# Kernel optimization log

Measured on AMD Instinct MI355X. Metric: run time of the kernel, lower is better.

## Reference

```python
import jax, jax.numpy as jnp
import numpy as np

E = 100000   # num edges
N = 50000    # num nodes (eg_idx, v, t triples)
B = 64       # num queries / subgraphs
D = 128      # n_dims_in
ID = 4 * D   # concat of 4 embeddings
OD = 2 * D   # G output dims
K = 1000     # max_edges per eg_idx


def setup_inputs() -> dict:
    key = jax.random.key(0)
    ks = jax.random.split(key, 12)
    eg_idx = jnp.sort(jax.random.randint(ks[0], (E,), 0, B)).astype(jnp.int32)
    node_i = jax.random.randint(ks[1], (E,), 0, N).astype(jnp.int32)
    node_j = jax.random.randint(ks[2], (E,), 0, N).astype(jnp.int32)
    node_score = jax.random.uniform(ks[3], (N,), dtype=jnp.float32)
    memorized_embedding = jax.random.normal(ks[4], (N, D), dtype=jnp.float32)
    rel_emb = jax.random.normal(ks[5], (E, D), dtype=jnp.float32)
    query_src_ts_emb = jax.random.normal(ks[6], (B, D), dtype=jnp.float32)
    query_rel_emb = jax.random.normal(ks[7], (B, D), dtype=jnp.float32)
    # G params: left/right dense init ~ N(0, sqrt(2/in)), center xavier-ish
    Wl = jax.random.normal(ks[8], (ID, OD), dtype=jnp.float32) * np.sqrt(2.0 / ID)
    Wr = jax.random.normal(ks[9], (ID, OD), dtype=jnp.float32) * np.sqrt(2.0 / ID)
    Wc = jax.random.normal(ks[10], (OD, OD), dtype=jnp.float32) * np.sqrt(2.0 / (OD + OD))
    bl = jnp.zeros((OD,), jnp.float32)
    br = jnp.zeros((OD,), jnp.float32)
    bc = jnp.zeros((OD,), jnp.float32)
    return dict(eg_idx=eg_idx, node_i=node_i, node_j=node_j, node_score=node_score,
                memorized_embedding=memorized_embedding, rel_emb=rel_emb,
                query_src_ts_emb=query_src_ts_emb, query_rel_emb=query_rel_emb,
                Wl=Wl, bl=bl, Wr=Wr, br=br, Wc=Wc, bc=bc, k=K)


def _segment_softmax(logits, seg, num_segments):
    m = jax.ops.segment_max(logits, seg, num_segments=num_segments)
    e = jnp.exp(logits - m[seg])
    s = jax.ops.segment_sum(e, seg, num_segments=num_segments)
    return e / s[seg]


def _topk_keep_mask(scores, group, num_groups, k):
    # keep edge iff its score ranks < k within its group (per-eg_idx topk)
    n = scores.shape[0]
    order = jnp.lexsort((-scores, group))          # sort by group asc, score desc
    sorted_group = group[order]
    counts = jax.ops.segment_sum(jnp.ones((n,), jnp.int32), group, num_segments=num_groups)
    starts = jnp.cumsum(counts) - counts           # exclusive cumsum: group start offsets
    rank_in_group = jnp.arange(n) - starts[sorted_group]
    keep_sorted = rank_in_group < k
    return jnp.zeros((n,), bool).at[order].set(keep_sorted)


def reference(eg_idx, node_i, node_j, node_score, memorized_embedding, rel_emb,
              query_src_ts_emb, query_rel_emb, Wl, bl, Wr, br, Wc, bc, k):
    num_nodes = memorized_embedding.shape[0]
    num_groups = query_src_ts_emb.shape[0]
    # gather per-edge embeddings
    hvi = memorized_embedding[node_i]              # [E, D]
    hvj = memorized_embedding[node_j]
    q_src = query_src_ts_emb[eg_idx]               # [E, D]
    q_rel = query_rel_emb[eg_idx]
    # G: bilinear MLP attention
    left_x = jnp.concatenate([hvi, rel_emb, q_src, q_rel], axis=-1)   # [E, 4D]
    right_x = jnp.concatenate([hvj, rel_emb, q_src, q_rel], axis=-1)
    l = jax.nn.leaky_relu(left_x @ Wl + bl)                           # [E, 2D]
    r = jax.nn.leaky_relu(right_x @ Wr + br) @ Wc + bc
    transition_logits = jnp.sum(l * r, axis=-1)                       # [E]
    # segment softmax over source node (eg_idx, vi, ti)
    soft = _segment_softmax(transition_logits, node_i, num_nodes)
    src_att = node_score[node_i]
    target_att = soft * src_att
    # per-eg_idx top-k pruning (keep mask instead of ragged slicing)
    keep = _topk_keep_mask(target_att, eg_idx, num_groups, k).astype(target_att.dtype)
    # sum aggregation: scatter soft * target_att into target nodes over kept edges
    updated_node_score = jax.ops.segment_sum(keep * soft * target_att, node_j,
                                             num_segments=num_nodes)
    return updated_node_score
```

## Files before the change

kernel.cpp:

```cpp
#include <hip/hip_runtime.h>

#define DD   128
#define ODIM 256
#define TE   32
#define TSLICE 16

__device__ __forceinline__ float leaky(float v) { return v > 0.f ? v : 0.01f * v; }

__global__ void k_query(const float* __restrict__ qs, const float* __restrict__ qr,
                        const float* __restrict__ Wl, const float* __restrict__ bl,
                        const float* __restrict__ Wr, const float* __restrict__ br,
                        float* __restrict__ Ql, float* __restrict__ Qr)
{
    const int g = blockIdx.x, t = threadIdx.x;
    float al = bl[t], ar = br[t];
    const float* qsg = qs + (size_t)g * DD;
    const float* qrg = qr + (size_t)g * DD;
    for (int k = 0; k < DD; ++k) {
        float a = qsg[k], b = qrg[k];
        al = fmaf(a, Wl[(size_t)(256 + k) * ODIM + t], al);
        al = fmaf(b, Wl[(size_t)(384 + k) * ODIM + t], al);
        ar = fmaf(a, Wr[(size_t)(256 + k) * ODIM + t], ar);
        ar = fmaf(b, Wr[(size_t)(384 + k) * ODIM + t], ar);
    }
    Ql[(size_t)g * ODIM + t] = al;
    Qr[(size_t)g * ODIM + t] = ar;
}

#define FMA4(dst, xc, wv, j)                                \
    dst[j][0] = fmaf(xc, wv.x, dst[j][0]);                  \
    dst[j][1] = fmaf(xc, wv.y, dst[j][1]);                  \
    dst[j][2] = fmaf(xc, wv.z, dst[j][2]);                  \
    dst[j][3] = fmaf(xc, wv.w, dst[j][3]);


__global__ __launch_bounds__(256, 2)
void k_nodepre(const float* __restrict__ me, const float* __restrict__ Wl,
               const float* __restrict__ Wr, float* __restrict__ Xl,
               float* __restrict__ Xr, int N)
{
    __shared__ float s_me[TE][DD];

    const int tx   = threadIdx.x;
    const int wave = tx >> 6;
    const int lane = tx & 63;
    const int colg = lane & 15;
    const int edgeg= lane >> 4;
    const int c0   = wave * 64 + colg * 4;
    const int eb   = edgeg * 8;
    const int n0   = blockIdx.x * TE;

    for (int it = tx; it < TE * DD / 4; it += 256) {
        int i  = it >> 5;
        int k4 = it & 31;
        float4 h = make_float4(0.f, 0.f, 0.f, 0.f);
        if (n0 + i < N) h = *(const float4*)(me + (size_t)(n0 + i) * DD + 4 * k4);
        *(float4*)(&s_me[i][(k4 ^ ((i >> 3) & 3)) << 2]) = h;
    }
    __syncthreads();

    float acc[8][4];
#pragma unroll
    for (int j = 0; j < 8; ++j) { acc[j][0] = acc[j][1] = acc[j][2] = acc[j][3] = 0.f; }
    for (int k4 = 0; k4 < 32; ++k4) {
        const float* wp = Wl + (size_t)(4 * k4) * ODIM + c0;
        float4 w0 = *(const float4*)(wp);
        float4 w1 = *(const float4*)(wp + ODIM);
        float4 w2 = *(const float4*)(wp + 2 * ODIM);
        float4 w3 = *(const float4*)(wp + 3 * ODIM);
        const int pc = (k4 ^ edgeg) << 2;
#pragma unroll
        for (int j = 0; j < 8; ++j) {
            float4 x = *(const float4*)(&s_me[eb + j][pc]);
            FMA4(acc, x.x, w0, j) FMA4(acc, x.y, w1, j) FMA4(acc, x.z, w2, j) FMA4(acc, x.w, w3, j)
        }
    }
#pragma unroll
    for (int j = 0; j < 8; ++j) {
        int n = n0 + eb + j;
        if (n < N)
            *(float4*)(Xl + (size_t)n * ODIM + c0) = make_float4(acc[j][0], acc[j][1], acc[j][2], acc[j][3]);
    }

#pragma unroll
    for (int j = 0; j < 8; ++j) { acc[j][0] = acc[j][1] = acc[j][2] = acc[j][3] = 0.f; }
    for (int k4 = 0; k4 < 32; ++k4) {
        const float* wp = Wr + (size_t)(4 * k4) * ODIM + c0;
        float4 w0 = *(const float4*)(wp);
        float4 w1 = *(const float4*)(wp + ODIM);
        float4 w2 = *(const float4*)(wp + 2 * ODIM);
        float4 w3 = *(const float4*)(wp + 3 * ODIM);
        const int pc = (k4 ^ edgeg) << 2;
#pragma unroll
        for (int j = 0; j < 8; ++j) {
            float4 x = *(const float4*)(&s_me[eb + j][pc]);
            FMA4(acc, x.x, w0, j) FMA4(acc, x.y, w1, j) FMA4(acc, x.z, w2, j) FMA4(acc, x.w, w3, j)
        }
    }
#pragma unroll
    for (int j = 0; j < 8; ++j) {
        int n = n0 + eb + j;
        if (n < N)
            *(float4*)(Xr + (size_t)n * ODIM + c0) = make_float4(acc[j][0], acc[j][1], acc[j][2], acc[j][3]);
    }
}

__global__ __launch_bounds__(256, 2)
void k_edge_logits_pre(const int* __restrict__ eg_idx, const int* __restrict__ node_i,
                       const int* __restrict__ node_j, const float* __restrict__ rel,
                       const float* __restrict__ Wl, const float* __restrict__ Wr,
                       const float* __restrict__ Wc, const float* __restrict__ bc,
                       const float* __restrict__ Ql, const float* __restrict__ Qr,
                       const float* __restrict__ Xl, const float* __restrict__ Xr,
                       float* __restrict__ logits, int E)
{
    __shared__ float s_a[TE][DD];
    __shared__ float s_b[TE][DD];
    __shared__ float s_red[4][TE];
    __shared__ int   s_ni[TE], s_nj[TE], s_g[TE];

    const int tx   = threadIdx.x;
    const int wave = tx >> 6;
    const int lane = tx & 63;
    const int colg = lane & 15;
    const int edgeg= lane >> 4;
    const int c0   = wave * 64 + colg * 4;
    const int eb   = edgeg * 8;
    const int e0   = blockIdx.x * TE;

    if (tx < TE) {
        int e = e0 + tx;
        s_ni[tx] = (e < E) ? node_i[e] : 0;
        s_nj[tx] = (e < E) ? node_j[e] : 0;
        s_g[tx]  = (e < E) ? eg_idx[e] : 0;
    }
    __syncthreads();

    for (int it = tx; it < TE * DD / 4; it += 256) {
        int i  = it >> 5;
        int k4 = it & 31;
        float4 v = make_float4(0.f, 0.f, 0.f, 0.f);
        if (e0 + i < E) v = *(const float4*)(rel + (size_t)(e0 + i) * DD + 4 * k4);
        *(float4*)(&s_a[i][(k4 ^ ((i >> 3) & 3)) << 2]) = v;
    }
    __syncthreads();

    float acc[8][4];
#pragma unroll
    for (int j = 0; j < 8; ++j) { acc[j][0] = acc[j][1] = acc[j][2] = acc[j][3] = 0.f; }

    for (int k4 = 0; k4 < 32; ++k4) {
        const float* wp = Wr + (size_t)(DD + 4 * k4) * ODIM + c0;
        float4 w0 = *(const float4*)(wp);
        float4 w1 = *(const float4*)(wp + ODIM);
        float4 w2 = *(const float4*)(wp + 2 * ODIM);
        float4 w3 = *(const float4*)(wp + 3 * ODIM);
        const int pc = (k4 ^ edgeg) << 2;
#pragma unroll
        for (int j = 0; j < 8; ++j) {
            float4 x = *(const float4*)(&s_a[eb + j][pc]);
            FMA4(acc, x.x, w0, j) FMA4(acc, x.y, w1, j) FMA4(acc, x.z, w2, j) FMA4(acc, x.w, w3, j)
        }
    }

#pragma unroll
    for (int j = 0; j < 8; ++j) {
        float4 xr = *(const float4*)(Xr + (size_t)s_nj[eb + j] * ODIM + c0);
        float4 q  = *(const float4*)(Qr + (size_t)s_g[eb + j] * ODIM + c0);
        acc[j][0] = leaky(acc[j][0] + xr.x + q.x);
        acc[j][1] = leaky(acc[j][1] + xr.y + q.y);
        acc[j][2] = leaky(acc[j][2] + xr.z + q.z);
        acc[j][3] = leaky(acc[j][3] + xr.w + q.w);
    }

    float uacc[8][4];
#pragma unroll
    for (int j = 0; j < 8; ++j) { uacc[j][0] = uacc[j][1] = uacc[j][2] = uacc[j][3] = 0.f; }

    if (wave < 2) {
        const int pc = ((wave * 16 + colg) ^ edgeg) << 2;
#pragma unroll
        for (int j = 0; j < 8; ++j)
            *(float4*)(&s_b[eb + j][pc]) = make_float4(acc[j][0], acc[j][1], acc[j][2], acc[j][3]);
    }
    __syncthreads();
    for (int k4 = 0; k4 < 32; ++k4) {
        const float* wp = Wc + (size_t)(4 * k4) * ODIM + c0;
        float4 w0 = *(const float4*)(wp);
        float4 w1 = *(const float4*)(wp + ODIM);
        float4 w2 = *(const float4*)(wp + 2 * ODIM);
        float4 w3 = *(const float4*)(wp + 3 * ODIM);
        const int pc = (k4 ^ edgeg) << 2;
#pragma unroll
        for (int j = 0; j < 8; ++j) {
            float4 x = *(const float4*)(&s_b[eb + j][pc]);
            FMA4(uacc, x.x, w0, j) FMA4(uacc, x.y, w1, j) FMA4(uacc, x.z, w2, j) FMA4(uacc, x.w, w3, j)
        }
    }
    __syncthreads();
    if (wave >= 2) {
        const int pc = ((wave * 16 + colg - 32) ^ edgeg) << 2;
#pragma unroll
        for (int j = 0; j < 8; ++j)
            *(float4*)(&s_b[eb + j][pc]) = make_float4(acc[j][0], acc[j][1], acc[j][2], acc[j][3]);
    }
    __syncthreads();
    for (int k4 = 0; k4 < 32; ++k4) {
        const float* wp = Wc + (size_t)(DD + 4 * k4) * ODIM + c0;
        float4 w0 = *(const float4*)(wp);
        float4 w1 = *(const float4*)(wp + ODIM);
        float4 w2 = *(const float4*)(wp + 2 * ODIM);
        float4 w3 = *(const float4*)(wp + 3 * ODIM);
        const int pc = (k4 ^ edgeg) << 2;
#pragma unroll
        for (int j = 0; j < 8; ++j) {
            float4 x = *(const float4*)(&s_b[eb + j][pc]);
            FMA4(uacc, x.x, w0, j) FMA4(uacc, x.y, w1, j) FMA4(uacc, x.z, w2, j) FMA4(uacc, x.w, w3, j)
        }
    }

    {
        float4 bcv = *(const float4*)(bc + c0);
#pragma unroll
        for (int j = 0; j < 8; ++j) {
            uacc[j][0] += bcv.x; uacc[j][1] += bcv.y;
            uacc[j][2] += bcv.z; uacc[j][3] += bcv.w;
        }
    }

#pragma unroll
    for (int j = 0; j < 8; ++j) { acc[j][0] = acc[j][1] = acc[j][2] = acc[j][3] = 0.f; }
    for (int k4 = 0; k4 < 32; ++k4) {
        const float* wp = Wl + (size_t)(DD + 4 * k4) * ODIM + c0;
        float4 w0 = *(const float4*)(wp);
        float4 w1 = *(const float4*)(wp + ODIM);
        float4 w2 = *(const float4*)(wp + 2 * ODIM);
        float4 w3 = *(const float4*)(wp + 3 * ODIM);
        const int pc = (k4 ^ edgeg) << 2;
#pragma unroll
        for (int j = 0; j < 8; ++j) {
            float4 x = *(const float4*)(&s_a[eb + j][pc]);
            FMA4(acc, x.x, w0, j) FMA4(acc, x.y, w1, j) FMA4(acc, x.z, w2, j) FMA4(acc, x.w, w3, j)
        }
    }

#pragma unroll
    for (int j = 0; j < 8; ++j) {
        float4 xl = *(const float4*)(Xl + (size_t)s_ni[eb + j] * ODIM + c0);
        float4 q  = *(const float4*)(Ql + (size_t)s_g[eb + j] * ODIM + c0);
        float p = leaky(acc[j][0] + xl.x + q.x) * uacc[j][0]
                + leaky(acc[j][1] + xl.y + q.y) * uacc[j][1]
                + leaky(acc[j][2] + xl.z + q.z) * uacc[j][2]
                + leaky(acc[j][3] + xl.w + q.w) * uacc[j][3];
        p += __shfl_xor(p, 1);
        p += __shfl_xor(p, 2);
        p += __shfl_xor(p, 4);
        p += __shfl_xor(p, 8);
        if (colg == 0) s_red[wave][eb + j] = p;
    }
    __syncthreads();
    if (tx < TE) {
        int e = e0 + tx;
        if (e < E)
            logits[e] = s_red[0][tx] + s_red[1][tx] + s_red[2][tx] + s_red[3][tx];
    }
}

__global__ __launch_bounds__(256, 2)
void k_edge_logits(const int* __restrict__ eg_idx, const int* __restrict__ node_i,
                   const int* __restrict__ node_j,
                   const float* __restrict__ me, const float* __restrict__ rel,
                   const float* __restrict__ Wl, const float* __restrict__ Wr,
                   const float* __restrict__ Wc, const float* __restrict__ bc,
                   const float* __restrict__ Ql, const float* __restrict__ Qr,
                   float* __restrict__ logits, int E)
{
    __shared__ float s_a[TE][DD];
    __shared__ float s_b[TE][DD];
    __shared__ int   s_ni[TE], s_nj[TE], s_g[TE];

    const int tx = threadIdx.x;
    const int cg = tx & 63;
    const int er = tx >> 6;
    const int c0 = cg << 2;
    const int e0 = blockIdx.x * TE;
    const int eb = er * 8;

    if (tx < TE) {
        int e = e0 + tx;
        s_ni[tx] = (e < E) ? node_i[e] : 0;
        s_nj[tx] = (e < E) ? node_j[e] : 0;
        s_g[tx]  = (e < E) ? eg_idx[e] : 0;
    }
    __syncthreads();

    for (int it = tx; it < TE * DD / 4; it += 256) {
        int i  = it >> 5;
        int kk = (it & 31) << 2;
        float4 v = make_float4(0.f, 0.f, 0.f, 0.f);
        float4 h = v;
        if (e0 + i < E) {
            v = *(const float4*)(rel + (size_t)(e0 + i) * DD + kk);
            h = *(const float4*)(me + (size_t)s_nj[i] * DD + kk);
        }
        *(float4*)(&s_a[i][kk]) = v;
        *(float4*)(&s_b[i][kk]) = h;
    }
    __syncthreads();

    float acc[8][4];
#pragma unroll
    for (int j = 0; j < 8; ++j) { acc[j][0] = acc[j][1] = acc[j][2] = acc[j][3] = 0.f; }

    for (int k = 0; k < DD; k += 4) {
        const float* wp = Wr + (size_t)k * ODIM + c0;
        float4 w0 = *(const float4*)(wp);
        float4 w1 = *(const float4*)(wp + ODIM);
        float4 w2 = *(const float4*)(wp + 2 * ODIM);
        float4 w3 = *(const float4*)(wp + 3 * ODIM);
#pragma unroll
        for (int j = 0; j < 8; ++j) {
            float4 x = *(const float4*)(&s_b[eb + j][k]);
            FMA4(acc, x.x, w0, j) FMA4(acc, x.y, w1, j) FMA4(acc, x.z, w2, j) FMA4(acc, x.w, w3, j)
        }
    }
    for (int k = 0; k < DD; k += 4) {
        const float* wp = Wr + (size_t)(DD + k) * ODIM + c0;
        float4 w0 = *(const float4*)(wp);
        float4 w1 = *(const float4*)(wp + ODIM);
        float4 w2 = *(const float4*)(wp + 2 * ODIM);
        float4 w3 = *(const float4*)(wp + 3 * ODIM);
#pragma unroll
        for (int j = 0; j < 8; ++j) {
            float4 x = *(const float4*)(&s_a[eb + j][k]);
            FMA4(acc, x.x, w0, j) FMA4(acc, x.y, w1, j) FMA4(acc, x.z, w2, j) FMA4(acc, x.w, w3, j)
        }
    }

#pragma unroll
    for (int j = 0; j < 8; ++j) {
        int g = s_g[eb + j];
        float4 q = *(const float4*)(Qr + (size_t)g * ODIM + c0);
        acc[j][0] = leaky(acc[j][0] + q.x);
        acc[j][1] = leaky(acc[j][1] + q.y);
        acc[j][2] = leaky(acc[j][2] + q.z);
        acc[j][3] = leaky(acc[j][3] + q.w);
    }

    float uacc[8][4];
#pragma unroll
    for (int j = 0; j < 8; ++j) { uacc[j][0] = uacc[j][1] = uacc[j][2] = uacc[j][3] = 0.f; }

    __syncthreads();
    if (c0 < DD) {
#pragma unroll
        for (int j = 0; j < 8; ++j)
            *(float4*)(&s_b[eb + j][c0]) = make_float4(acc[j][0], acc[j][1], acc[j][2], acc[j][3]);
    }
    __syncthreads();
    for (int k = 0; k < DD; k += 4) {
        const float* wp = Wc + (size_t)k * ODIM + c0;
        float4 w0 = *(const float4*)(wp);
        float4 w1 = *(const float4*)(wp + ODIM);
        float4 w2 = *(const float4*)(wp + 2 * ODIM);
        float4 w3 = *(const float4*)(wp + 3 * ODIM);
#pragma unroll
        for (int j = 0; j < 8; ++j) {
            float4 x = *(const float4*)(&s_b[eb + j][k]);
            FMA4(uacc, x.x, w0, j) FMA4(uacc, x.y, w1, j) FMA4(uacc, x.z, w2, j) FMA4(uacc, x.w, w3, j)
        }
    }
    __syncthreads();
    if (c0 >= DD) {
#pragma unroll
        for (int j = 0; j < 8; ++j)
            *(float4*)(&s_b[eb + j][c0 - DD]) = make_float4(acc[j][0], acc[j][1], acc[j][2], acc[j][3]);
    }
    __syncthreads();
    for (int k = 0; k < DD; k += 4) {
        const float* wp = Wc + (size_t)(DD + k) * ODIM + c0;
        float4 w0 = *(const float4*)(wp);
        float4 w1 = *(const float4*)(wp + ODIM);
        float4 w2 = *(const float4*)(wp + 2 * ODIM);
        float4 w3 = *(const float4*)(wp + 3 * ODIM);
#pragma unroll
        for (int j = 0; j < 8; ++j) {
            float4 x = *(const float4*)(&s_b[eb + j][k]);
            FMA4(uacc, x.x, w0, j) FMA4(uacc, x.y, w1, j) FMA4(uacc, x.z, w2, j) FMA4(uacc, x.w, w3, j)
        }
    }

    {
        float4 bcv = *(const float4*)(bc + c0);
#pragma unroll
        for (int j = 0; j < 8; ++j) {
            uacc[j][0] += bcv.x; uacc[j][1] += bcv.y;
            uacc[j][2] += bcv.z; uacc[j][3] += bcv.w;
        }
    }

    __syncthreads();
    for (int it = tx; it < TE * DD / 4; it += 256) {
        int i  = it >> 5;
        int kk = (it & 31) << 2;
        float4 h = make_float4(0.f, 0.f, 0.f, 0.f);
        if (e0 + i < E) h = *(const float4*)(me + (size_t)s_ni[i] * DD + kk);
        *(float4*)(&s_b[i][kk]) = h;
    }
    __syncthreads();

#pragma unroll
    for (int j = 0; j < 8; ++j) { acc[j][0] = acc[j][1] = acc[j][2] = acc[j][3] = 0.f; }

    for (int k = 0; k < DD; k += 4) {
        const float* wp = Wl + (size_t)k * ODIM + c0;
        float4 w0 = *(const float4*)(wp);
        float4 w1 = *(const float4*)(wp + ODIM);
        float4 w2 = *(const float4*)(wp + 2 * ODIM);
        float4 w3 = *(const float4*)(wp + 3 * ODIM);
#pragma unroll
        for (int j = 0; j < 8; ++j) {
            float4 x = *(const float4*)(&s_b[eb + j][k]);
            FMA4(acc, x.x, w0, j) FMA4(acc, x.y, w1, j) FMA4(acc, x.z, w2, j) FMA4(acc, x.w, w3, j)
        }
    }
    for (int k = 0; k < DD; k += 4) {
        const float* wp = Wl + (size_t)(DD + k) * ODIM + c0;
        float4 w0 = *(const float4*)(wp);
        float4 w1 = *(const float4*)(wp + ODIM);
        float4 w2 = *(const float4*)(wp + 2 * ODIM);
        float4 w3 = *(const float4*)(wp + 3 * ODIM);
#pragma unroll
        for (int j = 0; j < 8; ++j) {
            float4 x = *(const float4*)(&s_a[eb + j][k]);
            FMA4(acc, x.x, w0, j) FMA4(acc, x.y, w1, j) FMA4(acc, x.z, w2, j) FMA4(acc, x.w, w3, j)
        }
    }

#pragma unroll
    for (int j = 0; j < 8; ++j) {
        int g = s_g[eb + j];
        float4 q = *(const float4*)(Ql + (size_t)g * ODIM + c0);
        float p = leaky(acc[j][0] + q.x) * uacc[j][0]
                + leaky(acc[j][1] + q.y) * uacc[j][1]
                + leaky(acc[j][2] + q.z) * uacc[j][2]
                + leaky(acc[j][3] + q.w) * uacc[j][3];
#pragma unroll
        for (int off = 32; off > 0; off >>= 1) p += __shfl_down(p, off);
        if (cg == 0) {
            int e = e0 + eb + j;
            if (e < E) logits[e] = p;
        }
    }
}

__device__ __forceinline__ unsigned f32_enc(float f) {
    unsigned u = __float_as_uint(f);
    return (u & 0x80000000u) ? ~u : (u | 0x80000000u);
}
__device__ __forceinline__ float f32_dec(unsigned x) {
    return (x & 0x80000000u) ? __uint_as_float(x & 0x7fffffffu) : __uint_as_float(~x);
}

__global__ void k_segmax(const float* __restrict__ logits, const int* __restrict__ ni,
                         unsigned* __restrict__ segmax, int E)
{
    int e = blockIdx.x * 256 + threadIdx.x;
    if (e >= E) return;
    atomicMax(&segmax[ni[e]], f32_enc(logits[e]));
}

__global__ void k_expsum(const float* __restrict__ logits, const int* __restrict__ ni,
                         const unsigned* __restrict__ segmax,
                         float* __restrict__ eexp, float* __restrict__ segsum, int E)
{
    int e = blockIdx.x * 256 + threadIdx.x;
    if (e >= E) return;
    float m = f32_dec(segmax[ni[e]]);
    float v = expf(logits[e] - m);
    eexp[e] = v;
    atomicAdd(&segsum[ni[e]], v);
}

__global__ void k_soft(const float* __restrict__ eexp, const float* __restrict__ segsum,
                       const int* __restrict__ ni, const float* __restrict__ node_score,
                       float* __restrict__ soft, float* __restrict__ ta, int E)
{
    int e = blockIdx.x * 256 + threadIdx.x;
    if (e >= E) return;
    int n = ni[e];
    float s = eexp[e] / segsum[n];
    soft[e] = s;
    ta[e]   = s * node_score[n];
}

__global__ void k_starts(const int* __restrict__ eg, int E, int B, int* __restrict__ starts)
{
    int g = blockIdx.x * blockDim.x + threadIdx.x;
    if (g > B) return;
    int lo = 0, hi = E;
    while (lo < hi) { int mid = (lo + hi) >> 1; if (eg[mid] < g) lo = mid + 1; else hi = mid; }
    starts[g] = lo;
}

__global__ __launch_bounds__(256)
void k_topk(const int* __restrict__ starts, const int* __restrict__ node_j,
            const float* __restrict__ soft, const float* __restrict__ ta,
            const int* __restrict__ kptr, float* __restrict__ out)
{
    __shared__ float s_val[2048];
    const int g  = blockIdx.x / TSLICE;
    const int sl = blockIdx.x % TSLICE;
    const int gs = starts[g], ge = starts[g + 1];
    const int cnt = ge - gs;
    if (cnt <= 0) return;
    const int per = (cnt + TSLICE - 1) / TSLICE;
    const int c0  = sl * per;
    const int c1  = min(cnt, c0 + per);
    if (c0 >= cnt) return;
    const int K  = kptr[0];
    const int tx = threadIdx.x;

    for (int base = c0; base < c1; base += 256) {
        int   li  = base + tx;
        bool  act = li < c1;
        float mv  = act ? ta[gs + li] : 0.f;
        int   rank = 0;
        for (int t0 = 0; t0 < cnt; t0 += 2048) {
            int tlen = min(2048, cnt - t0);
            __syncthreads();
            for (int i = tx; i < tlen; i += 256) s_val[i] = ta[gs + t0 + i];
            __syncthreads();
            for (int i = 0; i < tlen; ++i) {
                float v  = s_val[i];
                int   gi = t0 + i;
                rank += (int)((v > mv) || (v == mv && gi < li));
            }
        }
        if (act && rank < K) {
            int e = gs + li;
            atomicAdd(&out[node_j[e]], soft[e] * ta[e]);
        }
    }
}

extern "C" void kernel_launch(void* const* d_in, const int* in_sizes, int n_in,
                              void* d_out, int out_size, void* d_ws, size_t ws_size,
                              hipStream_t stream)
{
    const int*   eg_idx     = (const int*)d_in[0];
    const int*   node_i     = (const int*)d_in[1];
    const int*   node_j     = (const int*)d_in[2];
    const float* node_score = (const float*)d_in[3];
    const float* me         = (const float*)d_in[4];
    const float* rel        = (const float*)d_in[5];
    const float* qs         = (const float*)d_in[6];
    const float* qr         = (const float*)d_in[7];
    const float* Wl         = (const float*)d_in[8];
    const float* bl         = (const float*)d_in[9];
    const float* Wr         = (const float*)d_in[10];
    const float* br         = (const float*)d_in[11];
    const float* Wc         = (const float*)d_in[12];
    const float* bc         = (const float*)d_in[13];
    const int*   kptr       = (const int*)d_in[14];

    const int E = in_sizes[0];
    const int N = in_sizes[3];
    const int B = in_sizes[6] / DD;

    float* ws      = (float*)d_ws;
    float* logits  = ws;
    float* eexp    = ws + (size_t)E;
    float* soft    = ws + 2 * (size_t)E;
    float* ta      = ws + 3 * (size_t)E;
    unsigned* segmax = (unsigned*)(ws + 4 * (size_t)E);
    float* segsum  = ws + 4 * (size_t)E + (size_t)N;
    float* Ql      = ws + 4 * (size_t)E + 2 * (size_t)N;
    float* Qr      = Ql + (size_t)B * ODIM;
    int*   starts  = (int*)(Qr + (size_t)B * ODIM);
    size_t base    = 4 * (size_t)E + 2 * (size_t)N + 2 * (size_t)B * ODIM + (size_t)(B + 1);
    float* Xl      = ws + base;
    float* Xr      = Xl + (size_t)N * ODIM;
    size_t needed  = (base + 2 * (size_t)N * ODIM) * sizeof(float);
    bool use_pre   = ws_size >= needed;

    hipMemsetAsync(d_out, 0, (size_t)N * sizeof(float), stream);
    hipMemsetAsync(segmax, 0, (size_t)2 * N * sizeof(float), stream);

    k_query<<<B, 256, 0, stream>>>(qs, qr, Wl, bl, Wr, br, Ql, Qr);
    if (use_pre) {
        k_nodepre<<<(N + TE - 1) / TE, 256, 0, stream>>>(me, Wl, Wr, Xl, Xr, N);
        k_edge_logits_pre<<<(E + TE - 1) / TE, 256, 0, stream>>>(eg_idx, node_i, node_j, rel,
                                                                 Wl, Wr, Wc, bc, Ql, Qr,
                                                                 Xl, Xr, logits, E);
    } else {
        k_edge_logits<<<(E + TE - 1) / TE, 256, 0, stream>>>(eg_idx, node_i, node_j, me, rel,
                                                             Wl, Wr, Wc, bc, Ql, Qr, logits, E);
    }
    int gE = (E + 255) / 256;
    k_segmax<<<gE, 256, 0, stream>>>(logits, node_i, segmax, E);
    k_expsum<<<gE, 256, 0, stream>>>(logits, node_i, segmax, eexp, segsum, E);
    k_soft<<<gE, 256, 0, stream>>>(eexp, segsum, node_i, node_score, soft, ta, E);
    k_starts<<<1, 128, 0, stream>>>(eg_idx, E, B, starts);
    k_topk<<<B * TSLICE, 256, 0, stream>>>(starts, node_j, soft, ta, kptr, (float*)d_out);
}
```

Baseline: 584.9 us.

## Retile edge-logits kernel to 64 edges per 512-thread block

The precomputed edge-logits kernel now handles 64 edges per block with 512 threads. Each wave covers 32 output columns across 8 edge groups instead of 64 columns across 4, so each weight float4 loaded from global memory is reused by twice as many edges. The shared-memory swizzle, the reduction shuffle and the cross-wave sum are adjusted to match. The cost is doubled shared memory per block and a larger block size, which may lower occupancy under launch_bounds(512,2).

```diff
diff --git a/kernel.cpp b/kernel.cpp
--- a/kernel.cpp
+++ b/kernel.cpp
@@ -3,6 +3,7 @@
 #define DD   128
 #define ODIM 256
 #define TE   32
+#define TE2  64
 #define TSLICE 16
 
 __device__ __forceinline__ float leaky(float v) { return v > 0.f ? v : 0.01f * v; }
@@ -33,7 +34,6 @@
     dst[j][2] = fmaf(xc, wv.z, dst[j][2]);                  \
     dst[j][3] = fmaf(xc, wv.w, dst[j][3]);
 
-
 __global__ __launch_bounds__(256, 2)
 void k_nodepre(const float* __restrict__ me, const float* __restrict__ Wl,
                const float* __restrict__ Wr, float* __restrict__ Xl,
@@ -68,7 +68,7 @@
         float4 w1 = *(const float4*)(wp + ODIM);
         float4 w2 = *(const float4*)(wp + 2 * ODIM);
         float4 w3 = *(const float4*)(wp + 3 * ODIM);
-        const int pc = (k4 ^ edgeg) << 2;
+        const int pc = ((k4 ^ edgeg) & 31) << 2;
 #pragma unroll
         for (int j = 0; j < 8; ++j) {
             float4 x = *(const float4*)(&s_me[eb + j][pc]);
@@ -90,7 +90,7 @@
         float4 w1 = *(const float4*)(wp + ODIM);
         float4 w2 = *(const float4*)(wp + 2 * ODIM);
         float4 w3 = *(const float4*)(wp + 3 * ODIM);
-        const int pc = (k4 ^ edgeg) << 2;
+        const int pc = ((k4 ^ edgeg) & 31) << 2;
 #pragma unroll
         for (int j = 0; j < 8; ++j) {
             float4 x = *(const float4*)(&s_me[eb + j][pc]);
@@ -105,7 +105,7 @@
     }
 }
 
-__global__ __launch_bounds__(256, 2)
+__global__ __launch_bounds__(512, 2)
 void k_edge_logits_pre(const int* __restrict__ eg_idx, const int* __restrict__ node_i,
                        const int* __restrict__ node_j, const float* __restrict__ rel,
                        const float* __restrict__ Wl, const float* __restrict__ Wr,
@@ -114,21 +114,21 @@
                        const float* __restrict__ Xl, const float* __restrict__ Xr,
                        float* __restrict__ logits, int E)
 {
-    __shared__ float s_a[TE][DD];
-    __shared__ float s_b[TE][DD];
-    __shared__ float s_red[4][TE];
-    __shared__ int   s_ni[TE], s_nj[TE], s_g[TE];
+    __shared__ float s_a[TE2][DD];
+    __shared__ float s_b[TE2][DD];
+    __shared__ float s_red[8][TE2];
+    __shared__ int   s_ni[TE2], s_nj[TE2], s_g[TE2];
 
     const int tx   = threadIdx.x;
     const int wave = tx >> 6;
     const int lane = tx & 63;
-    const int colg = lane & 15;
-    const int edgeg= lane >> 4;
-    const int c0   = wave * 64 + colg * 4;
+    const int colg = lane & 7;
+    const int edgeg= lane >> 3;
+    const int c0   = wave * 32 + colg * 4;
     const int eb   = edgeg * 8;
-    const int e0   = blockIdx.x * TE;
-
-    if (tx < TE) {
+    const int e0   = blockIdx.x * TE2;
+
+    if (tx < TE2) {
         int e = e0 + tx;
         s_ni[tx] = (e < E) ? node_i[e] : 0;
         s_nj[tx] = (e < E) ? node_j[e] : 0;
@@ -136,12 +136,12 @@
     }
     __syncthreads();
 
-    for (int it = tx; it < TE * DD / 4; it += 256) {
+    for (int it = tx; it < TE2 * DD / 4; it += 512) {
         int i  = it >> 5;
         int k4 = it & 31;
         float4 v = make_float4(0.f, 0.f, 0.f, 0.f);
         if (e0 + i < E) v = *(const float4*)(rel + (size_t)(e0 + i) * DD + 4 * k4);
-        *(float4*)(&s_a[i][(k4 ^ ((i >> 3) & 3)) << 2]) = v;
+        *(float4*)(&s_a[i][(k4 ^ ((i >> 3) & 7)) << 2]) = v;
     }
     __syncthreads();
 
@@ -155,7 +155,7 @@
         float4 w1 = *(const float4*)(wp + ODIM);
         float4 w2 = *(const float4*)(wp + 2 * ODIM);
         float4 w3 = *(const float4*)(wp + 3 * ODIM);
-        const int pc = (k4 ^ edgeg) << 2;
+        const int pc = ((k4 ^ edgeg) & 31) << 2;
 #pragma unroll
         for (int j = 0; j < 8; ++j) {
             float4 x = *(const float4*)(&s_a[eb + j][pc]);
@@ -177,8 +177,8 @@
 #pragma unroll
     for (int j = 0; j < 8; ++j) { uacc[j][0] = uacc[j][1] = uacc[j][2] = uacc[j][3] = 0.f; }
 
-    if (wave < 2) {
-        const int pc = ((wave * 16 + colg) ^ edgeg) << 2;
+    if (wave < 4) {
+        const int pc = (((wave * 8 + colg) ^ edgeg) & 31) << 2;
 #pragma unroll
         for (int j = 0; j < 8; ++j)
             *(float4*)(&s_b[eb + j][pc]) = make_float4(acc[j][0], acc[j][1], acc[j][2], acc[j][3]);
@@ -190,7 +190,7 @@
         float4 w1 = *(const float4*)(wp + ODIM);
         float4 w2 = *(const float4*)(wp + 2 * ODIM);
         float4 w3 = *(const float4*)(wp + 3 * ODIM);
-        const int pc = (k4 ^ edgeg) << 2;
+        const int pc = ((k4 ^ edgeg) & 31) << 2;
 #pragma unroll
         for (int j = 0; j < 8; ++j) {
             float4 x = *(const float4*)(&s_b[eb + j][pc]);
@@ -198,8 +198,8 @@
         }
     }
     __syncthreads();
-    if (wave >= 2) {
-        const int pc = ((wave * 16 + colg - 32) ^ edgeg) << 2;
+    if (wave >= 4) {
+        const int pc = ((((wave - 4) * 8 + colg) ^ edgeg) & 31) << 2;
 #pragma unroll
         for (int j = 0; j < 8; ++j)
             *(float4*)(&s_b[eb + j][pc]) = make_float4(acc[j][0], acc[j][1], acc[j][2], acc[j][3]);
@@ -211,7 +211,7 @@
         float4 w1 = *(const float4*)(wp + ODIM);
         float4 w2 = *(const float4*)(wp + 2 * ODIM);
         float4 w3 = *(const float4*)(wp + 3 * ODIM);
-        const int pc = (k4 ^ edgeg) << 2;
+        const int pc = ((k4 ^ edgeg) & 31) << 2;
 #pragma unroll
         for (int j = 0; j < 8; ++j) {
             float4 x = *(const float4*)(&s_b[eb + j][pc]);
@@ -236,7 +236,7 @@
         float4 w1 = *(const float4*)(wp + ODIM);
         float4 w2 = *(const float4*)(wp + 2 * ODIM);
         float4 w3 = *(const float4*)(wp + 3 * ODIM);
-        const int pc = (k4 ^ edgeg) << 2;
+        const int pc = ((k4 ^ edgeg) & 31) << 2;
 #pragma unroll
         for (int j = 0; j < 8; ++j) {
             float4 x = *(const float4*)(&s_a[eb + j][pc]);
@@ -255,14 +255,17 @@
         p += __shfl_xor(p, 1);
         p += __shfl_xor(p, 2);
         p += __shfl_xor(p, 4);
-        p += __shfl_xor(p, 8);
         if (colg == 0) s_red[wave][eb + j] = p;
     }
     __syncthreads();
-    if (tx < TE) {
+    if (tx < TE2) {
         int e = e0 + tx;
-        if (e < E)
-            logits[e] = s_red[0][tx] + s_red[1][tx] + s_red[2][tx] + s_red[3][tx];
+        if (e < E) {
+            float s = 0.f;
+#pragma unroll
+            for (int w = 0; w < 8; ++w) s += s_red[w][tx];
+            logits[e] = s;
+        }
     }
 }
 
@@ -275,18 +278,18 @@
                    const float* __restrict__ Ql, const float* __restrict__ Qr,
                    float* __restrict__ logits, int E)
 {
-    __shared__ float s_a[TE][DD];
-    __shared__ float s_b[TE][DD];
-    __shared__ int   s_ni[TE], s_nj[TE], s_g[TE];
+    __shared__ float s_a[32][DD];
+    __shared__ float s_b[32][DD];
+    __shared__ int   s_ni[32], s_nj[32], s_g[32];
 
     const int tx = threadIdx.x;
     const int cg = tx & 63;
     const int er = tx >> 6;
     const int c0 = cg << 2;
-    const int e0 = blockIdx.x * TE;
+    const int e0 = blockIdx.x * 32;
     const int eb = er * 8;
 
-    if (tx < TE) {
+    if (tx < 32) {
         int e = e0 + tx;
         s_ni[tx] = (e < E) ? node_i[e] : 0;
         s_nj[tx] = (e < E) ? node_j[e] : 0;
@@ -294,7 +297,7 @@
     }
     __syncthreads();
 
-    for (int it = tx; it < TE * DD / 4; it += 256) {
+    for (int it = tx; it < 32 * DD / 4; it += 256) {
         int i  = it >> 5;
         int kk = (it & 31) << 2;
         float4 v = make_float4(0.f, 0.f, 0.f, 0.f);
@@ -400,7 +403,7 @@
     }
 
     __syncthreads();
-    for (int it = tx; it < TE * DD / 4; it += 256) {
+    for (int it = tx; it < 32 * DD / 4; it += 256) {
         int i  = it >> 5;
         int kk = (it & 31) << 2;
         float4 h = make_float4(0.f, 0.f, 0.f, 0.f);
@@ -590,12 +593,12 @@
     k_query<<<B, 256, 0, stream>>>(qs, qr, Wl, bl, Wr, br, Ql, Qr);
     if (use_pre) {
         k_nodepre<<<(N + TE - 1) / TE, 256, 0, stream>>>(me, Wl, Wr, Xl, Xr, N);
-        k_edge_logits_pre<<<(E + TE - 1) / TE, 256, 0, stream>>>(eg_idx, node_i, node_j, rel,
-                                                                 Wl, Wr, Wc, bc, Ql, Qr,
-                                                                 Xl, Xr, logits, E);
+        k_edge_logits_pre<<<(E + TE2 - 1) / TE2, 512, 0, stream>>>(eg_idx, node_i, node_j, rel,
+                                                                   Wl, Wr, Wc, bc, Ql, Qr,
+                                                                   Xl, Xr, logits, E);
     } else {
-        k_edge_logits<<<(E + TE - 1) / TE, 256, 0, stream>>>(eg_idx, node_i, node_j, me, rel,
-                                                             Wl, Wr, Wc, bc, Ql, Qr, logits, E);
+        k_edge_logits<<<(E + 31) / 32, 256, 0, stream>>>(eg_idx, node_i, node_j, me, rel,
+                                                         Wl, Wr, Wc, bc, Ql, Qr, logits, E);
     }
     int gE = (E + 255) / 256;
     k_segmax<<<gE, 256, 0, stream>>>(logits, node_i, segmax, E);
```

Result: slower. 685.7 us (+17.2%).
